# Kernel tuning notes

Hardware: AMD Instinct MI355X
Metric: run time of the kernel (lower is better)

## Reference

```python
import jax, jax.numpy as jnp
import numpy as np

D_MODEL = 1024
NUM_HEADS = 16
HEAD_DIM = D_MODEL // NUM_HEADS
HIDDEN = 4096
EPS = 1e-10


def _layernorm(x, gamma, beta):
    mean = jnp.mean(x, axis=-1, keepdims=True)
    var = jnp.var(x, axis=-1, keepdims=True)  # unbiased=False
    return gamma * (x - mean) / jnp.sqrt(var + EPS) + beta


def setup_inputs() -> dict:
    key = jax.random.key(0)
    ks = jax.random.split(key, 16)
    s = 0.02
    d, h = D_MODEL, HIDDEN
    inp = {
        "x": jax.random.normal(ks[0], (4, 2048, d), dtype=jnp.float32),
        "Wq": jax.random.normal(ks[1], (d, d), dtype=jnp.float32) * s,
        "bq": jnp.zeros((d,), jnp.float32),
        "Wk": jax.random.normal(ks[2], (d, d), dtype=jnp.float32) * s,
        "bk": jnp.zeros((d,), jnp.float32),
        "Wv": jax.random.normal(ks[3], (d, d), dtype=jnp.float32) * s,
        "bv": jnp.zeros((d,), jnp.float32),
        "Wo": jax.random.normal(ks[4], (d, d), dtype=jnp.float32) * s,
        "bo": jnp.zeros((d,), jnp.float32),
        "W1": jax.random.normal(ks[5], (d, h), dtype=jnp.float32) * s,
        "b1": jnp.zeros((h,), jnp.float32),
        "W2": jax.random.normal(ks[6], (h, d), dtype=jnp.float32) * s,
        "b2": jnp.zeros((d,), jnp.float32),
        "gamma1": jnp.ones((d,), jnp.float32),
        "beta1": jnp.zeros((d,), jnp.float32),
        "gamma2": jnp.ones((d,), jnp.float32),
        "beta2": jnp.zeros((d,), jnp.float32),
    }
    return inp


def reference(x, Wq, bq, Wk, bk, Wv, bv, Wo, bo, W1, b1, W2, b2,
              gamma1, beta1, gamma2, beta2):
    B, S, D = x.shape
    H, hd = NUM_HEADS, HEAD_DIM
    scale = jnp.sqrt(jnp.float32(hd))

    # --- sublayer 1: self-attention on norm(x), residual add ---
    xn = _layernorm(x, gamma1, beta1)
    Q = (xn @ Wq + bq).reshape(B, S, H, hd).transpose(0, 2, 1, 3)  # [B,H,S,hd]
    K = (xn @ Wk + bk).reshape(B, S, H, hd).transpose(0, 2, 1, 3)
    V = (xn @ Wv + bv).reshape(B, S, H, hd).transpose(0, 2, 1, 3)
    scores = jnp.einsum("bhqd,bhkd->bhqk", Q, K) / scale  # [B,H,S,S]
    attn = jax.nn.softmax(scores, axis=-1)
    ctx = jnp.einsum("bhqk,bhkd->bhqd", attn, V)  # [B,H,S,hd]
    ctx = ctx.transpose(0, 2, 1, 3).reshape(B, S, D)
    x = x + (ctx @ Wo + bo)

    # --- sublayer 2: FFN on norm(x), residual add ---
    xn = _layernorm(x, gamma2, beta2)
    h = jax.nn.gelu(xn @ W1 + b1, approximate=False)  # torch F.gelu default = erf
    x = x + (h @ W2 + b2)
    return x
```

## Files before the change

### kernel.cpp

```cpp
#include <hip/hip_runtime.h>
#include <stdint.h>

#define D_MODEL 1024
#define HIDDEN  4096
#define SEQ     2048
#define NTOK    8192
#define NHEAD   16
#define HDIM    64

typedef unsigned short u16;
typedef __attribute__((ext_vector_type(8))) __bf16 bf16x8;
typedef __attribute__((ext_vector_type(4))) float f32x4;

__device__ __forceinline__ u16 f2bf(float f) {
  union { float f; unsigned u; } c; c.f = f;
  unsigned u = c.u + 0x7fffu + ((c.u >> 16) & 1u);
  return (u16)(u >> 16);
}

__device__ __forceinline__ void gload16(const void* g, void* l) {
  __builtin_amdgcn_global_load_lds((const __attribute__((address_space(1))) void*)g,
                                   (__attribute__((address_space(3))) void*)l, 16, 0, 0);
}

__global__ void transpose_cvt4(const float* __restrict__ A0, const float* __restrict__ A1,
                               const float* __restrict__ A2, const float* __restrict__ A3,
                               u16* __restrict__ O) {
  __shared__ float t[32][33];
  const int z = blockIdx.z;
  const float* W = (z == 0) ? A0 : (z == 1) ? A1 : (z == 2) ? A2 : A3;
  u16* Wt = O + ((size_t)z << 20);
  const int k0 = blockIdx.y * 32, n0 = blockIdx.x * 32;
  const int tx = threadIdx.x, ty = threadIdx.y;
#pragma unroll
  for (int p = 0; p < 4; ++p)
    t[ty + p * 8][tx] = W[(size_t)(k0 + ty + p * 8) * D_MODEL + n0 + tx];
  __syncthreads();
#pragma unroll
  for (int p = 0; p < 4; ++p) {
    const int n = ty + p * 8;
    Wt[(size_t)(n0 + n) * D_MODEL + k0 + tx] = f2bf(t[tx][n]);
  }
}

__global__ void transpose_cvt(const float* __restrict__ W, u16* __restrict__ Wt, int K, int N) {
  __shared__ float t[32][33];
  const int k0 = blockIdx.y * 32, n0 = blockIdx.x * 32;
  const int tx = threadIdx.x, ty = threadIdx.y;
#pragma unroll
  for (int p = 0; p < 4; ++p)
    t[ty + p * 8][tx] = W[(size_t)(k0 + ty + p * 8) * N + n0 + tx];
  __syncthreads();
#pragma unroll
  for (int p = 0; p < 4; ++p) {
    const int n = ty + p * 8;
    Wt[(size_t)(n0 + n) * K + k0 + tx] = f2bf(t[tx][n]);
  }
}

__global__ __launch_bounds__(256)
void ln_kernel(const float* __restrict__ x, const float* __restrict__ gamma,
               const float* __restrict__ beta, u16* __restrict__ out) {
  const int row = blockIdx.x;
  const int tid = threadIdx.x;
  const float4 v = ((const float4*)(x + (size_t)row * D_MODEL))[tid];
  float s = v.x + v.y + v.z + v.w;
  float q = v.x * v.x + v.y * v.y + v.z * v.z + v.w * v.w;
#pragma unroll
  for (int o = 32; o > 0; o >>= 1) { s += __shfl_down(s, o); q += __shfl_down(q, o); }
  __shared__ float ps[4], pq[4];
  const int wid = tid >> 6, lane = tid & 63;
  if (lane == 0) { ps[wid] = s; pq[wid] = q; }
  __syncthreads();
  s = ps[0] + ps[1] + ps[2] + ps[3];
  q = pq[0] + pq[1] + pq[2] + pq[3];
  const float mean = s * (1.0f / D_MODEL);
  const float var = q * (1.0f / D_MODEL) - mean * mean;
  const float rstd = rsqrtf(var + 1e-10f);
  const float4 gv = ((const float4*)gamma)[tid];
  const float4 bv = ((const float4*)beta)[tid];
  ushort4 o4;
  o4.x = f2bf((v.x - mean) * rstd * gv.x + bv.x);
  o4.y = f2bf((v.y - mean) * rstd * gv.y + bv.y);
  o4.z = f2bf((v.z - mean) * rstd * gv.z + bv.z);
  o4.w = f2bf((v.w - mean) * rstd * gv.w + bv.w);
  ((ushort4*)(out + (size_t)row * D_MODEL))[tid] = o4;
}

template <int EPI, int KPY, int KPX>
__global__ __launch_bounds__(256, 3)
void gemm97(const u16* __restrict__ A, const u16* __restrict__ Bt,
            const float* __restrict__ bias, const float* __restrict__ bias2,
            const float* __restrict__ res, void* __restrict__ outp, void* __restrict__ outp2,
            int M, int N, int K) {
  __shared__ u16 As[128 * 32];
  __shared__ u16 Bs[128 * 32];
  const int tid = threadIdx.x;
  const int wid = tid >> 6, lane = tid & 63;
  const int g = lane >> 4, lr = lane & 15;
  const int wm = (wid & 1) << 6, wn = (wid >> 1) << 6;

  const int xcd = blockIdx.x & 7, l = blockIdx.x >> 3;
  int bx, by;
  if (KPY > 0) { by = xcd * KPY + (l % KPY); bx = l / KPY; }
  else         { bx = xcd * KPX + (l % KPX); by = l / KPX; }
  const int m0 = by * 128, n0 = bx * 128;

  const int NT = K >> 5;

  const int r0 = tid >> 2;
  const int c0 = ((tid & 3) ^ (r0 & 3)) << 3;
  const u16* pA0 = A + (size_t)(m0 + r0) * K + c0;
  const u16* pA1 = A + (size_t)(m0 + r0 + 64) * K + c0;
  const u16* pB0 = Bt + (size_t)(n0 + r0) * K + c0;
  const u16* pB1 = Bt + (size_t)(n0 + r0 + 64) * K + c0;
  const int d0 = (tid & 192) * 16;

  f32x4 acc[4][4] = {};
  const int cx = (g ^ (lr & 3)) << 3;

  for (int t = 0; t < NT; ++t) {
    __syncthreads();
    gload16(pA0, (char*)As + d0);
    gload16(pA1, (char*)As + d0 + 4096);
    gload16(pB0, (char*)Bs + d0);
    gload16(pB1, (char*)Bs + d0 + 4096);
    pA0 += 32; pA1 += 32; pB0 += 32; pB1 += 32;
    __syncthreads();

    bf16x8 af[4], bfr[4];
#pragma unroll
    for (int f = 0; f < 4; ++f) {
      af[f] = *(const bf16x8*)(As + (wm + f * 16 + lr) * 32 + cx);
      bfr[f] = *(const bf16x8*)(Bs + (wn + f * 16 + lr) * 32 + cx);
    }
    __builtin_amdgcn_s_setprio(1);
#pragma unroll
    for (int mf = 0; mf < 4; ++mf)
#pragma unroll
      for (int nf = 0; nf < 4; ++nf)
        acc[mf][nf] = __builtin_amdgcn_mfma_f32_16x16x32_bf16(af[mf], bfr[nf], acc[mf][nf], 0, 0, 0);
    __builtin_amdgcn_s_setprio(0);
  }

#pragma unroll
  for (int mf = 0; mf < 4; ++mf)
#pragma unroll
    for (int nf = 0; nf < 4; ++nf) {
      const int gn = n0 + wn + nf * 16 + lr;
      const int gm = m0 + wm + mf * 16 + 4 * g;
#pragma unroll
      for (int r = 0; r < 4; ++r) {
        const float av = acc[mf][nf][r];
        if (EPI == 0) {
          ((u16*)outp)[(size_t)(gm + r) * N + gn] = f2bf(av + bias[gn]);
        } else if (EPI == 1) {
          const size_t idx = (size_t)(gm + r) * N + gn;
          ((float*)outp)[idx] = av + bias[gn] + res[idx];
        } else if (EPI == 2) {
          const float v = av + bias[gn];
          ((u16*)outp)[(size_t)(gm + r) * N + gn] =
              f2bf(0.5f * v * (1.0f + erff(v * 0.7071067811865475f)));
        } else if (EPI == 3) {
          const int gn_p = (gn & ~63) | ((gn & 15) << 2) | ((gn >> 4) & 3);
          ((u16*)outp)[(size_t)(gm + r) * N + gn_p] = f2bf(av + bias[gm + r]);
        } else {
          const int side = gn >> 10, col = gn & 1023;
          u16* o = (u16*)(side ? outp2 : outp);
          float t_ = av + (side ? bias2[col] : bias[col]);
          if (!side) t_ *= 0.18033688011112042f;
          o[(size_t)(gm + r) * 1024 + col] = f2bf(t_);
        }
      }
    }
}

__global__ __launch_bounds__(256, 4)
void attn_kernel(const u16* __restrict__ Q, const u16* __restrict__ K,
                 const u16* __restrict__ Vt, u16* __restrict__ ctxo) {
  const int L = blockIdx.x;
  const int q0 = ((L >> 3) & 15) * 128;
  const int bh = ((L >> 7) << 3) | (L & 7);
  const int b = bh >> 4, h = bh & 15;
  const int tid = threadIdx.x, wid = tid >> 6, lane = tid & 63;
  const int g = lane >> 4, lr = lane & 15;
  const size_t base = ((size_t)b * SEQ) * D_MODEL + h * HDIM;
  const size_t vbase = ((size_t)h * HDIM) * NTOK + (size_t)b * SEQ;

#define AST 76
  __shared__ u16 Ks[64 * AST];
  __shared__ u16 Vts[64 * AST];
  __shared__ u16 Ps[128 * AST];

  const int qw = wid * 32;

#pragma unroll
  for (int i = 0; i < 4; ++i) {
    const int ch = tid + 256 * i, row = ch >> 3, j = ch & 7;
    *(bf16x8*)(Ps + row * AST + j * 8) =
        *(const bf16x8*)(Q + base + (size_t)(q0 + row) * D_MODEL + j * 8);
  }
  __syncthreads();
  bf16x8 aq[2][2];
#pragma unroll
  for (int qf = 0; qf < 2; ++qf)
#pragma unroll
    for (int ks = 0; ks < 2; ++ks)
      aq[qf][ks] = *(const bf16x8*)(Ps + (qw + qf * 16 + lr) * AST + ks * 32 + g * 8);

  f32x4 o[2][4] = {};
  float lrun[2][4] = {};

  for (int kv0 = 0; kv0 < SEQ; kv0 += 64) {
    __syncthreads();
#pragma unroll
    for (int i = 0; i < 2; ++i) {
      const int row = (tid >> 3) + i * 32, j = tid & 7;
      *(bf16x8*)(Ks + row * AST + j * 8) =
          *(const bf16x8*)(K + base + (size_t)(kv0 + row) * D_MODEL + j * 8);
      *(bf16x8*)(Vts + row * AST + j * 8) =
          *(const bf16x8*)(Vt + vbase + (size_t)row * NTOK + kv0 + j * 8);
    }
    __syncthreads();

    f32x4 s[2][4] = {};
    __builtin_amdgcn_s_setprio(1);
#pragma unroll
    for (int ks = 0; ks < 2; ++ks)
#pragma unroll
      for (int kf = 0; kf < 4; ++kf) {
        const bf16x8 bk = *(const bf16x8*)(Ks + (kf * 16 + lr) * AST + ks * 32 + g * 8);
#pragma unroll
        for (int qf = 0; qf < 2; ++qf)
          s[qf][kf] = __builtin_amdgcn_mfma_f32_16x16x32_bf16(aq[qf][ks], bk, s[qf][kf], 0, 0, 0);
      }
    __builtin_amdgcn_s_setprio(0);

#pragma unroll
    for (int qf = 0; qf < 2; ++qf)
#pragma unroll
      for (int r = 0; r < 4; ++r) {
        float p0, p1, p2, p3;
        asm("v_exp_f32 %0, %1" : "=v"(p0) : "v"(s[qf][0][r]));
        asm("v_exp_f32 %0, %1" : "=v"(p1) : "v"(s[qf][1][r]));
        asm("v_exp_f32 %0, %1" : "=v"(p2) : "v"(s[qf][2][r]));
        asm("v_exp_f32 %0, %1" : "=v"(p3) : "v"(s[qf][3][r]));
        lrun[qf][r] += (p0 + p1) + (p2 + p3);
        unsigned lo, hi;
        asm("v_cvt_pk_bf16_f32 %0, %1, %2" : "=v"(lo) : "v"(p0), "v"(p1));
        asm("v_cvt_pk_bf16_f32 %0, %1, %2" : "=v"(hi) : "v"(p2), "v"(p3));
        *(uint2*)(Ps + (qw + qf * 16 + 4 * g + r) * AST + lr * 4) = make_uint2(lo, hi);
      }
    asm volatile("s_waitcnt lgkmcnt(0)" ::: "memory");

    __builtin_amdgcn_s_setprio(1);
#pragma unroll
    for (int ks = 0; ks < 2; ++ks) {
      bf16x8 pf[2];
#pragma unroll
      for (int qf = 0; qf < 2; ++qf)
        pf[qf] = *(const bf16x8*)(Ps + (qw + qf * 16 + lr) * AST + ks * 32 + g * 8);
#pragma unroll
      for (int df = 0; df < 4; ++df) {
        const bf16x8 vf = *(const bf16x8*)(Vts + (df * 16 + lr) * AST + ks * 32 + g * 8);
#pragma unroll
        for (int qf = 0; qf < 2; ++qf)
          o[qf][df] = __builtin_amdgcn_mfma_f32_16x16x32_bf16(pf[qf], vf, o[qf][df], 0, 0, 0);
      }
    }
    __builtin_amdgcn_s_setprio(0);
  }

#pragma unroll
  for (int off = 1; off < 16; off <<= 1)
#pragma unroll
    for (int qf = 0; qf < 2; ++qf)
#pragma unroll
      for (int r = 0; r < 4; ++r)
        lrun[qf][r] += __shfl_xor(lrun[qf][r], off);

#pragma unroll
  for (int qf = 0; qf < 2; ++qf)
#pragma unroll
    for (int r = 0; r < 4; ++r) {
      const float rinv = 1.0f / lrun[qf][r];
      const int qrow = q0 + qw + qf * 16 + 4 * g + r;
#pragma unroll
      for (int df = 0; df < 4; ++df)
        ctxo[base + (size_t)qrow * D_MODEL + df * 16 + lr] = f2bf(o[qf][df][r] * rinv);
    }
#undef AST
}

extern "C" void kernel_launch(void* const* d_in, const int* in_sizes, int n_in,
                              void* d_out, int out_size, void* d_ws, size_t ws_size,
                              hipStream_t stream) {
  const float* x  = (const float*)d_in[0];
  const float* Wq = (const float*)d_in[1];
  const float* bq = (const float*)d_in[2];
  const float* Wk = (const float*)d_in[3];
  const float* bk = (const float*)d_in[4];
  const float* Wv = (const float*)d_in[5];
  const float* bv = (const float*)d_in[6];
  const float* Wo = (const float*)d_in[7];
  const float* bo = (const float*)d_in[8];
  const float* W1 = (const float*)d_in[9];
  const float* b1 = (const float*)d_in[10];
  const float* W2 = (const float*)d_in[11];
  const float* b2 = (const float*)d_in[12];
  const float* gamma1 = (const float*)d_in[13];
  const float* beta1  = (const float*)d_in[14];
  const float* gamma2 = (const float*)d_in[15];
  const float* beta2  = (const float*)d_in[16];
  float* out = (float*)d_out;

  const size_t M1 = 1u << 20;
  u16* w   = (u16*)d_ws;
  u16* WtQ = w;
  u16* WtV = w + 2 * M1;
  u16* WtO = w + 3 * M1;
  u16* Wt1 = w + 4 * M1;
  u16* Wt2 = w + 8 * M1;
  u16* xn  = w + 12 * M1;
  u16* Qb  = w + 20 * M1;
  u16* Kb  = w + 28 * M1;
  u16* Vtb = w + 36 * M1;
  u16* ctx = w + 44 * M1;
  u16* hb  = w + 20 * M1;
  float* x1 = (float*)(w + 52 * M1);

  const dim3 tb(32, 8);
  transpose_cvt4<<<dim3(32, 32, 4), tb, 0, stream>>>(Wq, Wk, Wv, Wo, WtQ);
  transpose_cvt<<<dim3(HIDDEN / 32, D_MODEL / 32), tb, 0, stream>>>(W1, Wt1, D_MODEL, HIDDEN);
  transpose_cvt<<<dim3(D_MODEL / 32, HIDDEN / 32), tb, 0, stream>>>(W2, Wt2, HIDDEN, D_MODEL);

  ln_kernel<<<NTOK, 256, 0, stream>>>(x, gamma1, beta1, xn);

  gemm97<6, 8, 0><<<1024, 256, 0, stream>>>(xn, WtQ, bq, bk, nullptr, Qb, Kb,
                                            NTOK, 2048, D_MODEL);
  gemm97<3, 1, 0><<<512, 256, 0, stream>>>(WtV, xn, bv, nullptr, nullptr, Vtb, nullptr,
                                           D_MODEL, NTOK, D_MODEL);

  attn_kernel<<<1024, 256, 0, stream>>>(Qb, Kb, Vtb, ctx);

  gemm97<1, 8, 0><<<512, 256, 0, stream>>>(ctx, WtO, bo, nullptr, x, x1, nullptr,
                                           NTOK, D_MODEL, D_MODEL);

  ln_kernel<<<NTOK, 256, 0, stream>>>(x1, gamma2, beta2, xn);

  gemm97<2, 8, 0><<<2048, 256, 0, stream>>>(xn, Wt1, b1, nullptr, nullptr, hb, nullptr,
                                            NTOK, HIDDEN, D_MODEL);
  gemm97<1, 8, 0><<<512, 256, 0, stream>>>(hb, Wt2, b2, nullptr, x1, out, nullptr,
                                           NTOK, D_MODEL, HIDDEN);
}
```

Before: 398.7 us.

## Double GEMM K-tile to 64 with 8-way swizzle and prefetch K/V in attention

```diff
diff --git a/kernel.cpp b/kernel.cpp
--- a/kernel.cpp
+++ b/kernel.cpp
@@ -89,12 +89,12 @@
 
 template <int EPI, int KPY, int KPX>
 __global__ __launch_bounds__(256, 3)
-void gemm97(const u16* __restrict__ A, const u16* __restrict__ Bt,
+void gemm64(const u16* __restrict__ A, const u16* __restrict__ Bt,
             const float* __restrict__ bias, const float* __restrict__ bias2,
             const float* __restrict__ res, void* __restrict__ outp, void* __restrict__ outp2,
             int M, int N, int K) {
-  __shared__ u16 As[128 * 32];
-  __shared__ u16 Bs[128 * 32];
+  __shared__ u16 As[128 * 64];
+  __shared__ u16 Bs[128 * 64];
   const int tid = threadIdx.x;
   const int wid = tid >> 6, lane = tid & 63;
   const int g = lane >> 4, lr = lane & 15;
@@ -106,41 +106,51 @@
   else         { bx = xcd * KPX + (l % KPX); by = l / KPX; }
   const int m0 = by * 128, n0 = bx * 128;
 
-  const int NT = K >> 5;
-
-  const int r0 = tid >> 2;
-  const int c0 = ((tid & 3) ^ (r0 & 3)) << 3;
-  const u16* pA0 = A + (size_t)(m0 + r0) * K + c0;
-  const u16* pA1 = A + (size_t)(m0 + r0 + 64) * K + c0;
-  const u16* pB0 = Bt + (size_t)(n0 + r0) * K + c0;
-  const u16* pB1 = Bt + (size_t)(n0 + r0 + 64) * K + c0;
-  const int d0 = (tid & 192) * 16;
+  const int NT = K >> 6;
+
+  const int r0 = tid >> 3;
+  const int csw = ((tid & 7) ^ (r0 & 7)) << 3;
+  const u16* pA[4];
+  const u16* pB[4];
+#pragma unroll
+  for (int i = 0; i < 4; ++i) {
+    pA[i] = A + (size_t)(m0 + r0 + i * 32) * K + csw;
+    pB[i] = Bt + (size_t)(n0 + r0 + i * 32) * K + csw;
+  }
+  const int db = (tid & 192) * 16;
 
   f32x4 acc[4][4] = {};
-  const int cx = (g ^ (lr & 3)) << 3;
 
   for (int t = 0; t < NT; ++t) {
     __syncthreads();
-    gload16(pA0, (char*)As + d0);
-    gload16(pA1, (char*)As + d0 + 4096);
-    gload16(pB0, (char*)Bs + d0);
-    gload16(pB1, (char*)Bs + d0 + 4096);
-    pA0 += 32; pA1 += 32; pB0 += 32; pB1 += 32;
+#pragma unroll
+    for (int i = 0; i < 4; ++i) {
+      gload16(pA[i], (char*)As + db + i * 4096);
+      gload16(pB[i], (char*)Bs + db + i * 4096);
+      pA[i] += 64; pB[i] += 64;
+    }
     __syncthreads();
 
-    bf16x8 af[4], bfr[4];
-#pragma unroll
-    for (int f = 0; f < 4; ++f) {
-      af[f] = *(const bf16x8*)(As + (wm + f * 16 + lr) * 32 + cx);
-      bfr[f] = *(const bf16x8*)(Bs + (wn + f * 16 + lr) * 32 + cx);
-    }
-    __builtin_amdgcn_s_setprio(1);
-#pragma unroll
-    for (int mf = 0; mf < 4; ++mf)
-#pragma unroll
-      for (int nf = 0; nf < 4; ++nf)
-        acc[mf][nf] = __builtin_amdgcn_mfma_f32_16x16x32_bf16(af[mf], bfr[nf], acc[mf][nf], 0, 0, 0);
-    __builtin_amdgcn_s_setprio(0);
+#pragma unroll
+    for (int ks = 0; ks < 2; ++ks) {
+      bf16x8 af[4], bfr[4];
+#pragma unroll
+      for (int f = 0; f < 4; ++f) {
+        const int ra = wm + f * 16 + lr;
+        const int rb = wn + f * 16 + lr;
+        const int co = ((ks * 4 + g) ^ (lr & 7)) * 8;
+        af[f] = *(const bf16x8*)(As + ra * 64 + co);
+        bfr[f] = *(const bf16x8*)(Bs + rb * 64 + co);
+      }
+      __builtin_amdgcn_s_setprio(1);
+#pragma unroll
+      for (int mf = 0; mf < 4; ++mf)
+#pragma unroll
+        for (int nf = 0; nf < 4; ++nf)
+          acc[mf][nf] =
+              __builtin_amdgcn_mfma_f32_16x16x32_bf16(af[mf], bfr[nf], acc[mf][nf], 0, 0, 0);
+      __builtin_amdgcn_s_setprio(0);
+    }
   }
 
 #pragma unroll
@@ -208,20 +218,36 @@
     for (int ks = 0; ks < 2; ++ks)
       aq[qf][ks] = *(const bf16x8*)(Ps + (qw + qf * 16 + lr) * AST + ks * 32 + g * 8);
 
+  const int r0 = tid >> 3, j0 = (tid & 7) << 3;
+  const u16* pK0 = K + base + (size_t)r0 * D_MODEL + j0;
+  const u16* pK1 = pK0 + (size_t)32 * D_MODEL;
+  const u16* pV0 = Vt + vbase + (size_t)r0 * NTOK + j0;
+  const u16* pV1 = pV0 + (size_t)32 * NTOK;
+  u16* dK0 = Ks + r0 * AST + j0;
+  u16* dK1 = dK0 + 32 * AST;
+  u16* dV0 = Vts + r0 * AST + j0;
+  u16* dV1 = dV0 + 32 * AST;
+
+  bf16x8 kr0 = *(const bf16x8*)pK0, kr1 = *(const bf16x8*)pK1;
+  bf16x8 vr0 = *(const bf16x8*)pV0, vr1 = *(const bf16x8*)pV1;
+
   f32x4 o[2][4] = {};
   float lrun[2][4] = {};
 
   for (int kv0 = 0; kv0 < SEQ; kv0 += 64) {
     __syncthreads();
-#pragma unroll
-    for (int i = 0; i < 2; ++i) {
-      const int row = (tid >> 3) + i * 32, j = tid & 7;
-      *(bf16x8*)(Ks + row * AST + j * 8) =
-          *(const bf16x8*)(K + base + (size_t)(kv0 + row) * D_MODEL + j * 8);
-      *(bf16x8*)(Vts + row * AST + j * 8) =
-          *(const bf16x8*)(Vt + vbase + (size_t)row * NTOK + kv0 + j * 8);
-    }
+    *(bf16x8*)dK0 = kr0;
+    *(bf16x8*)dK1 = kr1;
+    *(bf16x8*)dV0 = vr0;
+    *(bf16x8*)dV1 = vr1;
     __syncthreads();
+
+    if (kv0 + 64 < SEQ) {
+      pK0 += (size_t)64 * D_MODEL; pK1 += (size_t)64 * D_MODEL;
+      pV0 += 64; pV1 += 64;
+      kr0 = *(const bf16x8*)pK0; kr1 = *(const bf16x8*)pK1;
+      vr0 = *(const bf16x8*)pV0; vr1 = *(const bf16x8*)pV1;
+    }
 
     f32x4 s[2][4] = {};
     __builtin_amdgcn_s_setprio(1);
@@ -336,20 +362,20 @@
 
   ln_kernel<<<NTOK, 256, 0, stream>>>(x, gamma1, beta1, xn);
 
-  gemm97<6, 8, 0><<<1024, 256, 0, stream>>>(xn, WtQ, bq, bk, nullptr, Qb, Kb,
+  gemm64<6, 8, 0><<<1024, 256, 0, stream>>>(xn, WtQ, bq, bk, nullptr, Qb, Kb,
                                             NTOK, 2048, D_MODEL);
-  gemm97<3, 1, 0><<<512, 256, 0, stream>>>(WtV, xn, bv, nullptr, nullptr, Vtb, nullptr,
+  gemm64<3, 0, 8><<<512, 256, 0, stream>>>(WtV, xn, bv, nullptr, nullptr, Vtb, nullptr,
                                            D_MODEL, NTOK, D_MODEL);
 
   attn_kernel<<<1024, 256, 0, stream>>>(Qb, Kb, Vtb, ctx);
 
-  gemm97<1, 8, 0><<<512, 256, 0, stream>>>(ctx, WtO, bo, nullptr, x, x1, nullptr,
+  gemm64<1, 8, 0><<<512, 256, 0, stream>>>(ctx, WtO, bo, nullptr, x, x1, nullptr,
                                            NTOK, D_MODEL, D_MODEL);
 
   ln_kernel<<<NTOK, 256, 0, stream>>>(x1, gamma2, beta2, xn);
 
-  gemm97<2, 8, 0><<<2048, 256, 0, stream>>>(xn, Wt1, b1, nullptr, nullptr, hb, nullptr,
+  gemm64<2, 8, 0><<<2048, 256, 0, stream>>>(xn, Wt1, b1, nullptr, nullptr, hb, nullptr,
                                             NTOK, HIDDEN, D_MODEL);
-  gemm97<1, 8, 0><<<512, 256, 0, stream>>>(hb, Wt2, b2, nullptr, x1, out, nullptr,
+  gemm64<1, 8, 0><<<512, 256, 0, stream>>>(hb, Wt2, b2, nullptr, x1, out, nullptr,
                                            NTOK, D_MODEL, HIDDEN);
 }
```

New measurement: 371.0 us. -7.0%, faster.
